# Performance work log

Hardware: AMD Instinct MI355X
Metric: run time of the kernel (lower is better)

## Reference

```python
import jax, jax.numpy as jnp
import numpy as np
import math

NUM_PARAM = 9
STRIDE = 1
BN_EPS = 1e-5


def _make_p_n(N):
    # matches LDConv._get_p_n: irregular kernel offset grid of N points
    base = round(math.sqrt(N))
    rows = N // base
    mod = N % base
    gx, gy = np.meshgrid(np.arange(rows), np.arange(base), indexing='ij')
    px, py = gx.ravel(), gy.ravel()
    if mod > 0:
        mx, my = np.meshgrid(np.arange(rows, rows + 1), np.arange(mod), indexing='ij')
        px = np.concatenate([px, mx.ravel()])
        py = np.concatenate([py, my.ravel()])
    return jnp.asarray(np.concatenate([px, py]), jnp.float32).reshape(1, 2 * N, 1, 1)


def _conv2d_same(x, w, stride, pad):
    return jax.lax.conv_general_dilated(
        x, w, (stride, stride), [(pad, pad), (pad, pad)],
        dimension_numbers=('NCHW', 'OIHW', 'NCHW'))


def _gather(xf, q, W, N):
    # xf: (b,c,H*W); q: (b,h,w,2N) int indices -> (b,c,h,w,N)
    idx = q[..., :N] * W + q[..., N:]
    return jax.vmap(lambda xb, ib: xb[:, ib])(xf, idx)


def setup_inputs() -> dict:
    key = jax.random.key(0)
    ks = jax.random.split(key, 3)
    B, C, H, W = 8, 128, 64, 64
    outc = 256
    x = jax.random.normal(ks[0], (B, C, H, W), jnp.float32)
    # p_conv init: uniform(-1e-4, 1e-4) weights, zero bias (per the torch module)
    p_conv_w = jax.random.uniform(ks[1], (2 * NUM_PARAM, C, 3, 3), jnp.float32, -1e-4, 1e-4)
    p_conv_b = jnp.zeros((2 * NUM_PARAM,), jnp.float32)
    conv_w = jax.random.normal(ks[2], (outc, C, NUM_PARAM, 1), jnp.float32) / math.sqrt(C * NUM_PARAM)
    bn_gamma = jnp.ones((outc,), jnp.float32)
    bn_beta = jnp.zeros((outc,), jnp.float32)
    bn_mean = jnp.zeros((outc,), jnp.float32)
    bn_var = jnp.ones((outc,), jnp.float32)
    return dict(x=x, p_conv_w=p_conv_w, p_conv_b=p_conv_b, conv_w=conv_w,
                bn_gamma=bn_gamma, bn_beta=bn_beta, bn_mean=bn_mean, bn_var=bn_var)


def reference(x, p_conv_w, p_conv_b, conv_w, bn_gamma, bn_beta, bn_mean, bn_var):
    N = NUM_PARAM
    B, C, H, W = x.shape
    offset = _conv2d_same(x, p_conv_w, STRIDE, 1) + p_conv_b[None, :, None, None]  # (b,2N,h,w)
    h, w = offset.shape[2], offset.shape[3]
    gx, gy = jnp.meshgrid(jnp.arange(0, h * STRIDE, STRIDE),
                          jnp.arange(0, w * STRIDE, STRIDE), indexing='ij')
    p_0 = jnp.concatenate([jnp.broadcast_to(gx, (1, N, h, w)),
                           jnp.broadcast_to(gy, (1, N, h, w))], axis=1).astype(x.dtype)
    p = (p_0 + _make_p_n(N) + offset).transpose(0, 2, 3, 1)  # (b,h,w,2N)

    q_lt = jnp.floor(jax.lax.stop_gradient(p))
    q_rb = q_lt + 1
    clampi = lambda q: jnp.concatenate([jnp.clip(q[..., :N], 0, H - 1),
                                        jnp.clip(q[..., N:], 0, W - 1)], -1).astype(jnp.int32)
    q_lt = clampi(q_lt)
    q_rb = clampi(q_rb)
    q_lb = jnp.concatenate([q_lt[..., :N], q_rb[..., N:]], -1)
    q_rt = jnp.concatenate([q_rb[..., :N], q_lt[..., N:]], -1)
    p = jnp.concatenate([jnp.clip(p[..., :N], 0, H - 1),
                         jnp.clip(p[..., N:], 0, W - 1)], -1)
    f = lambda q: q.astype(p.dtype)
    g_lt = (1 + (f(q_lt[..., :N]) - p[..., :N])) * (1 + (f(q_lt[..., N:]) - p[..., N:]))
    g_rb = (1 - (f(q_rb[..., :N]) - p[..., :N])) * (1 - (f(q_rb[..., N:]) - p[..., N:]))
    g_lb = (1 + (f(q_lb[..., :N]) - p[..., :N])) * (1 - (f(q_lb[..., N:]) - p[..., N:]))
    g_rt = (1 - (f(q_rt[..., :N]) - p[..., :N])) * (1 + (f(q_rt[..., N:]) - p[..., N:]))

    xf = x.reshape(B, C, H * W)
    x_off = (g_lt[:, None] * _gather(xf, q_lt, W, N)
             + g_rb[:, None] * _gather(xf, q_rb, W, N)
             + g_lb[:, None] * _gather(xf, q_lb, W, N)
             + g_rt[:, None] * _gather(xf, q_rt, W, N))  # (b,c,h,w,N)
    # rearrange 'b c h w n -> b c (h n) w'
    x_off = x_off.transpose(0, 1, 2, 4, 3).reshape(B, C, h * N, w)

    y = jax.lax.conv_general_dilated(x_off, conv_w, (N, 1), 'VALID',
                                     dimension_numbers=('NCHW', 'OIHW', 'NCHW'))
    scale = (bn_gamma / jnp.sqrt(bn_var + BN_EPS))[None, :, None, None]
    y = (y - bn_mean[None, :, None, None]) * scale + bn_beta[None, :, None, None]
    return y * jax.nn.sigmoid(y)  # SiLU
```

## Files before the change

kernel.cpp:

```cpp
#include <hip/hip_runtime.h>
#include <hip/hip_bf16.h>
#include <cstdint>

#define B_   8
#define C_   128
#define H_   64
#define W_   64
#define NPT  9
#define OC   256
#define K_   (C_*NPT)
#define HW   (H_*W_)
#define MTOT (B_*HW)

typedef __attribute__((ext_vector_type(8))) short short8;
typedef __attribute__((ext_vector_type(4))) float f32x4;
typedef __attribute__((ext_vector_type(4))) unsigned int u32x4;
typedef __attribute__((ext_vector_type(2))) unsigned int u32x2;

static __device__ __forceinline__ unsigned short f2bf(float f) {
    union { float f; unsigned u; } a; a.f = f;
    unsigned r = a.u + 0x7fffu + ((a.u >> 16) & 1u);
    return (unsigned short)(r >> 16);
}
static __device__ __forceinline__ float bf2f(unsigned short u) {
    union { unsigned u; float f; } a; a.u = ((unsigned)u) << 16;
    return a.f;
}

__global__ __launch_bounds__(512) void k_offset2(const float* __restrict__ x,
                                                 const float* __restrict__ pw,
                                                 const float* __restrict__ pb,
                                                 float* __restrict__ off) {
    __shared__ __align__(16) float wlds[128 * 180];
    __shared__ float red[8 * 64 * 19];
    int b = blockIdx.x >> 5;
    int i0 = (blockIdx.x & 31) * 2;
    int t = threadIdx.x;

    for (int idx = t; idx < 128 * 9 * 18; idx += 512) {
        int c = idx / 162;
        int r = idx - c * 162;
        int tap = r / 18;
        int o = r - tap * 18;
        wlds[c * 180 + tap * 20 + o] = pw[o * K_ + c * 9 + tap];
    }
    __syncthreads();

    int j = t & 63;
    int cg = t >> 6;
    const float* xb = x + (size_t)b * C_ * HW;
    float acc[2][18];
#pragma unroll
    for (int p = 0; p < 2; ++p)
#pragma unroll
        for (int o = 0; o < 18; ++o) acc[p][o] = 0.f;

    for (int cc = 0; cc < 16; ++cc) {
        int c = cg * 16 + cc;
        const float* xc = xb + (size_t)c * HW;
        float xv[4][3];
#pragma unroll
        for (int q = 0; q < 4; ++q) {
            int row = i0 - 1 + q;
            if (row >= 0 && row < H_) {
                const float* xr = xc + row * W_;
                xv[q][1] = xr[j];
                xv[q][0] = (j > 0)  ? xr[j - 1] : 0.f;
                xv[q][2] = (j < 63) ? xr[j + 1] : 0.f;
            } else {
                xv[q][0] = xv[q][1] = xv[q][2] = 0.f;
            }
        }
        const float* wc = wlds + c * 180;
#pragma unroll
        for (int tap = 0; tap < 9; ++tap) {
            const int kh = tap / 3, kw = tap % 3;
            float w18[20];
            *(f32x4*)(w18 + 0)  = *(const f32x4*)(wc + tap * 20 + 0);
            *(f32x4*)(w18 + 4)  = *(const f32x4*)(wc + tap * 20 + 4);
            *(f32x4*)(w18 + 8)  = *(const f32x4*)(wc + tap * 20 + 8);
            *(f32x4*)(w18 + 12) = *(const f32x4*)(wc + tap * 20 + 12);
            *(f32x4*)(w18 + 16) = *(const f32x4*)(wc + tap * 20 + 16);
#pragma unroll
            for (int p = 0; p < 2; ++p) {
                float xval = xv[p + kh][kw];
#pragma unroll
                for (int o = 0; o < 18; ++o) acc[p][o] += w18[o] * xval;
            }
        }
    }

#pragma unroll
    for (int p = 0; p < 2; ++p) {
        __syncthreads();
#pragma unroll
        for (int o = 0; o < 18; ++o) red[(cg * 64 + j) * 19 + o] = acc[p][o];
        __syncthreads();
        for (int e = t; e < 64 * 18; e += 512) {
            int jj = e / 18, o = e - jj * 18;
            float s = 0.f;
#pragma unroll
            for (int g = 0; g < 8; ++g) s += red[(g * 64 + jj) * 19 + o];
            off[(((size_t)b * 18 + o) * H_ + (i0 + p)) * W_ + jj] = s + pb[o];
        }
    }
}

__global__ __launch_bounds__(256) void k_prepw(const float* __restrict__ cw,
                                               const float* __restrict__ gam,
                                               const float* __restrict__ bet,
                                               const float* __restrict__ mu,
                                               const float* __restrict__ var,
                                               __hip_bfloat16* __restrict__ wbf,
                                               float* __restrict__ bias) {
    int idx = blockIdx.x * 256 + threadIdx.x;
    int oc = idx / K_;
    int r = idx - oc * K_;
    int n = r >> 7;
    int c = r & 127;
    float sc = gam[oc] * rsqrtf(var[oc] + 1e-5f);
    wbf[idx] = __float2bfloat16(cw[oc * K_ + c * NPT + n] * sc);
    if (blockIdx.x == 0 && threadIdx.x < OC) {
        int o = threadIdx.x;
        float s = gam[o] * rsqrtf(var[o] + 1e-5f);
        bias[o] = bet[o] - mu[o] * s;
    }
}

__global__ __launch_bounds__(256) void k_gather(const float* __restrict__ x,
                                                const float* __restrict__ off,
                                                __hip_bfloat16* __restrict__ xoff) {
    __shared__ __align__(16) char sx[98368 + 64];
    __shared__ __align__(16) f32x4 swt[1152];
    __shared__ uint32_t scrd[1152];
    int b = blockIdx.x >> 5;
    int i0 = (blockIdx.x & 31) * 2;
    int t = threadIdx.x;

    const float* xb = x + (size_t)b * C_ * HW;
#pragma unroll 4
    for (int it = 0; it < 48; ++it) {
        int q = it * 256 + t;
        int c = q / 96;
        int rem = q - c * 96;
        int s = rem >> 4;
        int c4 = rem & 15;
        int gr = min(63, max(0, i0 - 1 + s));
        f32x4 v = *(const f32x4*)(xb + (size_t)c * HW + gr * 64 + c4 * 4);
        u32x2 pk;
        pk.x = (uint32_t)f2bf(v.x) | ((uint32_t)f2bf(v.y) << 16);
        pk.y = (uint32_t)f2bf(v.z) | ((uint32_t)f2bf(v.w) << 16);
        *(u32x2*)(sx + c * 768 + ((c >> 6) << 6) + s * 128 + c4 * 8) = pk;
    }

    for (int task = t; task < 1152; task += 256) {
        int n = task >> 7;
        int pxl = task & 127;
        int i = i0 + (pxl >> 6);
        int j = pxl & 63;
        const float* ob = off + (((size_t)b * 18 + n) * H_ + i) * W_ + j;
        float ox = ob[0];
        float oy = ob[9 * HW];
        float pxf = (float)(i + n / 3) + ox;
        float pyf = (float)(j + n % 3) + oy;
        float fx = floorf(pxf), fy = floorf(pyf);
        int r0 = max(0, min(63, (int)fx));
        int r1 = max(0, min(63, (int)fx + 1));
        int c0 = max(0, min(63, (int)fy));
        int c1 = max(0, min(63, (int)fy + 1));
        float pxc = fminf(fmaxf(pxf, 0.f), 63.f);
        float pyc = fminf(fmaxf(pyf, 0.f), 63.f);
        float ax = 1.f + ((float)r0 - pxc);
        float bx = 1.f - ((float)r1 - pxc);
        float ay = 1.f + ((float)c0 - pyc);
        float by = 1.f - ((float)c1 - pyc);
        f32x4 w; w.x = ax * ay; w.y = bx * by; w.z = ax * by; w.w = bx * ay;
        swt[task] = w;
        int s0 = max(0, min(5, r0 - (i0 - 1)));
        int s1 = max(0, min(5, r1 - (i0 - 1)));
        scrd[task] = (uint32_t)(s0 | (s1 << 8) | (c0 << 16) | (c1 << 24));
    }
    __syncthreads();

    int wv = t >> 6;
    int h = (t >> 5) & 1;
    int pxl = wv * 32 + (t & 31);
    const char* sxh = sx + h * (64 * 768 + 64);
    char* ob = (char*)xoff + ((size_t)blockIdx.x * 128 + pxl) * (K_ * 2) + h * 128;
    for (int n = 0; n < 9; ++n) {
        f32x4 w = swt[n * 128 + pxl];
        uint32_t crd = scrd[n * 128 + pxl];
        int s0 = crd & 255, s1 = (crd >> 8) & 255, c0 = (crd >> 16) & 255, c1 = crd >> 24;
        int o00 = s0 * 128 + c0 * 2;
        int o11 = s1 * 128 + c1 * 2;
        int o01 = s0 * 128 + c1 * 2;
        int o10 = s1 * 128 + c0 * 2;
        for (int cg = 0; cg < 8; ++cg) {
            u32x4 pk;
#pragma unroll
            for (int u2 = 0; u2 < 4; ++u2) {
                unsigned short r[2];
#pragma unroll
                for (int e = 0; e < 2; ++e) {
                    int cl = cg * 8 + u2 * 2 + e;
                    const char* base = sxh + cl * 768;
                    float v = w.x * bf2f(*(const unsigned short*)(base + o00))
                            + w.y * bf2f(*(const unsigned short*)(base + o11))
                            + w.z * bf2f(*(const unsigned short*)(base + o01))
                            + w.w * bf2f(*(const unsigned short*)(base + o10));
                    r[e] = f2bf(v);
                }
                pk[u2] = (uint32_t)r[0] | ((uint32_t)r[1] << 16);
            }
            *(u32x4*)(ob + n * 256 + cg * 16) = pk;
        }
    }
}

#define BM 128
#define BN 128
#define BK 64
#define NTILES (K_ / BK)

__global__ __launch_bounds__(256) void k_gemm(const __hip_bfloat16* __restrict__ xoff,
                                              const __hip_bfloat16* __restrict__ wbf,
                                              const float* __restrict__ bias,
                                              float* __restrict__ out) {
    __shared__ __align__(16) char smem[2 * 2 * BM * BK * 2];
    int tid = threadIdx.x;
    int mt = blockIdx.x >> 1;
    int nt = blockIdx.x & 1;
    const char* Ab = (const char*)xoff + (size_t)mt * BM * (K_ * 2);
    const char* Bb = (const char*)wbf  + (size_t)nt * BN * (K_ * 2);

    auto stage = [&](int buf, int kt) {
        const int winByte = kt * (BK * 2);
#pragma unroll
        for (int q = 0; q < 4; ++q) {
            int ch = q * 256 + tid;
            int row = ch >> 3, slot = ch & 7;
            int srcoff = row * (K_ * 2) + winByte + ((slot * 16) ^ ((row & 7) << 4));
            __builtin_amdgcn_global_load_lds(
                (const __attribute__((address_space(1))) uint32_t*)(Ab + srcoff),
                (__attribute__((address_space(3))) uint32_t*)(smem + buf * 32768 + ch * 16),
                16, 0, 0);
        }
#pragma unroll
        for (int q = 0; q < 4; ++q) {
            int ch = q * 256 + tid;
            int row = ch >> 3, slot = ch & 7;
            int srcoff = row * (K_ * 2) + winByte + ((slot * 16) ^ ((row & 7) << 4));
            __builtin_amdgcn_global_load_lds(
                (const __attribute__((address_space(1))) uint32_t*)(Bb + srcoff),
                (__attribute__((address_space(3))) uint32_t*)(smem + buf * 32768 + 16384 + ch * 16),
                16, 0, 0);
        }
    };

    int wv = tid >> 6, lane = tid & 63;
    int wr = wv >> 1, wc = wv & 1;
    int lrow = lane & 15, lg = lane >> 4;

    f32x4 zero = {0.f, 0.f, 0.f, 0.f};
    f32x4 acc[4][4];
#pragma unroll
    for (int m = 0; m < 4; ++m)
#pragma unroll
        for (int n = 0; n < 4; ++n) acc[m][n] = zero;

    stage(0, 0);
    for (int kt = 0; kt < NTILES; ++kt) {
        if (kt + 1 < NTILES) stage((kt + 1) & 1, kt + 1);
        __syncthreads();
        const char* sa = smem + (kt & 1) * 32768;
        const char* sb = sa + 16384;
#pragma unroll
        for (int kk = 0; kk < 2; ++kk) {
            short8 afr[4], bfr[4];
#pragma unroll
            for (int m = 0; m < 4; ++m) {
                int row = wr * 64 + m * 16 + lrow;
                int byt = kk * 64 + lg * 16;
                afr[m] = *(const short8*)(sa + row * 128 + (byt ^ ((row & 7) << 4)));
            }
#pragma unroll
            for (int n = 0; n < 4; ++n) {
                int row = wc * 64 + n * 16 + lrow;
                int byt = kk * 64 + lg * 16;
                bfr[n] = *(const short8*)(sb + row * 128 + (byt ^ ((row & 7) << 4)));
            }
#pragma unroll
            for (int m = 0; m < 4; ++m)
#pragma unroll
                for (int n = 0; n < 4; ++n)
                    acc[m][n] = __builtin_amdgcn_mfma_f32_16x16x32_bf16(afr[m], bfr[n], acc[m][n], 0, 0, 0);
        }
        __syncthreads();
    }

#pragma unroll
    for (int n = 0; n < 4; ++n) {
        int oc = nt * BN + wc * 64 + n * 16 + lrow;
        float bs = bias[oc];
#pragma unroll
        for (int m = 0; m < 4; ++m) {
            int pxb = mt * BM + wr * 64 + m * 16 + lg * 4;
#pragma unroll
            for (int r = 0; r < 4; ++r) {
                int px = pxb + r;
                float v = acc[m][n][r] + bs;
                float sv = v / (1.f + __expf(-v));
                out[((size_t)(px >> 12) * OC + oc) * HW + (px & 4095)] = sv;
            }
        }
    }
}

extern "C" void kernel_launch(void* const* d_in, const int* in_sizes, int n_in,
                              void* d_out, int out_size, void* d_ws, size_t ws_size,
                              hipStream_t stream) {
    const float* x   = (const float*)d_in[0];
    const float* pw  = (const float*)d_in[1];
    const float* pb  = (const float*)d_in[2];
    const float* cw  = (const float*)d_in[3];
    const float* gam = (const float*)d_in[4];
    const float* bet = (const float*)d_in[5];
    const float* mu  = (const float*)d_in[6];
    const float* var = (const float*)d_in[7];
    float* out = (float*)d_out;

    char* ws = (char*)d_ws;
    float* off           = (float*)ws;
    __hip_bfloat16* wbf  = (__hip_bfloat16*)(ws + 2359296);
    float* bias          = (float*)(ws + 2949120);
    __hip_bfloat16* xoff = (__hip_bfloat16*)(ws + 2950144);

    hipLaunchKernelGGL(k_offset2, dim3(256),  dim3(512), 0, stream, x, pw, pb, off);
    hipLaunchKernelGGL(k_prepw,   dim3(1152), dim3(256), 0, stream, cw, gam, bet, mu, var, wbf, bias);
    hipLaunchKernelGGL(k_gather,  dim3(256),  dim3(256), 0, stream, x, off, xoff);
    hipLaunchKernelGGL(k_gemm,    dim3(512),  dim3(256), 0, stream, xoff, wbf, bias, out);
}
```

Measured before the change: 108.6 us.

## Restructure gather to channel-contiguous LDS layout and widen GEMM tile to full OC

The gather kernel now handles one output row per block and stores the 5-row input halo in LDS as pixel-major, channel-contiguous bf16 with an XOR swizzle. Each bilinear corner can then be read as 8-channel vector loads instead of scalar per-channel loads, and the per-pixel weights and coordinates stay in registers rather than going through LDS. The GEMM moves to 512-thread blocks covering all 256 output channels per 128-pixel tile, so each activation tile is loaded only once. The trade-off is fewer GEMM blocks (256), more LDS per block, and per-element scattered LDS stores when building the transposed halo.

```diff
diff --git a/kernel.cpp b/kernel.cpp
--- a/kernel.cpp
+++ b/kernel.cpp
@@ -130,39 +130,44 @@
 __global__ __launch_bounds__(256) void k_gather(const float* __restrict__ x,
                                                 const float* __restrict__ off,
                                                 __hip_bfloat16* __restrict__ xoff) {
-    __shared__ __align__(16) char sx[98368 + 64];
-    __shared__ __align__(16) f32x4 swt[1152];
-    __shared__ uint32_t scrd[1152];
-    int b = blockIdx.x >> 5;
-    int i0 = (blockIdx.x & 31) * 2;
+    __shared__ __align__(16) char sx[5 * 64 * 256];
+    int b = blockIdx.x >> 6;
+    int i = blockIdx.x & 63;
     int t = threadIdx.x;
 
     const float* xb = x + (size_t)b * C_ * HW;
 #pragma unroll 4
-    for (int it = 0; it < 48; ++it) {
-        int q = it * 256 + t;
-        int c = q / 96;
-        int rem = q - c * 96;
-        int s = rem >> 4;
-        int c4 = rem & 15;
-        int gr = min(63, max(0, i0 - 1 + s));
+    for (int it = 0; it < 40; ++it) {
+        int ch = it * 256 + t;
+        int c4 = ch & 15;
+        int c  = (ch >> 4) & 127;
+        int s  = ch >> 11;
+        int gr = min(63, max(0, i - 1 + s));
         f32x4 v = *(const f32x4*)(xb + (size_t)c * HW + gr * 64 + c4 * 4);
-        u32x2 pk;
-        pk.x = (uint32_t)f2bf(v.x) | ((uint32_t)f2bf(v.y) << 16);
-        pk.y = (uint32_t)f2bf(v.z) | ((uint32_t)f2bf(v.w) << 16);
-        *(u32x2*)(sx + c * 768 + ((c >> 6) << 6) + s * 128 + c4 * 8) = pk;
-    }
-
-    for (int task = t; task < 1152; task += 256) {
-        int n = task >> 7;
-        int pxl = task & 127;
-        int i = i0 + (pxl >> 6);
-        int j = pxl & 63;
-        const float* ob = off + (((size_t)b * 18 + n) * H_ + i) * W_ + j;
-        float ox = ob[0];
-        float oy = ob[9 * HW];
-        float pxf = (float)(i + n / 3) + ox;
-        float pyf = (float)(j + n % 3) + oy;
+        int g = c >> 3;
+        int sub = (c & 7) * 2;
+#pragma unroll
+        for (int k2 = 0; k2 < 4; ++k2) {
+            int col = c4 * 4 + k2;
+            *(unsigned short*)(sx + (s * 64 + col) * 256 + (((g ^ (col & 15)) << 4) + sub)) = f2bf(v[k2]);
+        }
+    }
+
+    int j = t & 63;
+    int cg = t >> 6;
+    float oxv[9], oyv[9];
+    const float* ob = off + (((size_t)b * 18) * H_ + i) * W_ + j;
+#pragma unroll
+    for (int n = 0; n < 9; ++n) {
+        oxv[n] = ob[(size_t)n * HW];
+        oyv[n] = ob[(size_t)(n + 9) * HW];
+    }
+    __syncthreads();
+
+    char* outp = (char*)xoff + ((size_t)blockIdx.x * 64 + j) * (K_ * 2) + cg * 64;
+    for (int n = 0; n < 9; ++n) {
+        float pxf = (float)(i + n / 3) + oxv[n];
+        float pyf = (float)(j + n % 3) + oyv[n];
         float fx = floorf(pxf), fy = floorf(pyf);
         int r0 = max(0, min(63, (int)fx));
         int r1 = max(0, min(63, (int)fx + 1));
@@ -174,91 +179,81 @@
         float bx = 1.f - ((float)r1 - pxc);
         float ay = 1.f + ((float)c0 - pyc);
         float by = 1.f - ((float)c1 - pyc);
-        f32x4 w; w.x = ax * ay; w.y = bx * by; w.z = ax * by; w.w = bx * ay;
-        swt[task] = w;
-        int s0 = max(0, min(5, r0 - (i0 - 1)));
-        int s1 = max(0, min(5, r1 - (i0 - 1)));
-        scrd[task] = (uint32_t)(s0 | (s1 << 8) | (c0 << 16) | (c1 << 24));
-    }
-    __syncthreads();
-
-    int wv = t >> 6;
-    int h = (t >> 5) & 1;
-    int pxl = wv * 32 + (t & 31);
-    const char* sxh = sx + h * (64 * 768 + 64);
-    char* ob = (char*)xoff + ((size_t)blockIdx.x * 128 + pxl) * (K_ * 2) + h * 128;
-    for (int n = 0; n < 9; ++n) {
-        f32x4 w = swt[n * 128 + pxl];
-        uint32_t crd = scrd[n * 128 + pxl];
-        int s0 = crd & 255, s1 = (crd >> 8) & 255, c0 = (crd >> 16) & 255, c1 = crd >> 24;
-        int o00 = s0 * 128 + c0 * 2;
-        int o11 = s1 * 128 + c1 * 2;
-        int o01 = s0 * 128 + c1 * 2;
-        int o10 = s1 * 128 + c0 * 2;
-        for (int cg = 0; cg < 8; ++cg) {
+        float w00 = ax * ay, w11 = bx * by, w01 = ax * by, w10 = bx * ay;
+        int s0 = max(0, min(4, r0 - (i - 1)));
+        int s1 = max(0, min(4, r1 - (i - 1)));
+        const char* b00 = sx + (s0 * 64 + c0) * 256;
+        const char* b11 = sx + (s1 * 64 + c1) * 256;
+        const char* b01 = sx + (s0 * 64 + c1) * 256;
+        const char* b10 = sx + (s1 * 64 + c0) * 256;
+        int x0m = (c0 & 15) << 4, x1m = (c1 & 15) << 4;
+#pragma unroll
+        for (int u = 0; u < 4; ++u) {
+            int gb = (cg * 4 + u) << 4;
+            short8 t00 = *(const short8*)(b00 + (gb ^ x0m));
+            short8 t11 = *(const short8*)(b11 + (gb ^ x1m));
+            short8 t01 = *(const short8*)(b01 + (gb ^ x1m));
+            short8 t10 = *(const short8*)(b10 + (gb ^ x0m));
             u32x4 pk;
 #pragma unroll
-            for (int u2 = 0; u2 < 4; ++u2) {
-                unsigned short r[2];
+            for (int p2 = 0; p2 < 4; ++p2) {
+                unsigned short rr[2];
 #pragma unroll
                 for (int e = 0; e < 2; ++e) {
-                    int cl = cg * 8 + u2 * 2 + e;
-                    const char* base = sxh + cl * 768;
-                    float v = w.x * bf2f(*(const unsigned short*)(base + o00))
-                            + w.y * bf2f(*(const unsigned short*)(base + o11))
-                            + w.z * bf2f(*(const unsigned short*)(base + o01))
-                            + w.w * bf2f(*(const unsigned short*)(base + o10));
-                    r[e] = f2bf(v);
+                    int ei = p2 * 2 + e;
+                    float v = w00 * bf2f((unsigned short)t00[ei])
+                            + w11 * bf2f((unsigned short)t11[ei])
+                            + w01 * bf2f((unsigned short)t01[ei])
+                            + w10 * bf2f((unsigned short)t10[ei]);
+                    rr[e] = f2bf(v);
                 }
-                pk[u2] = (uint32_t)r[0] | ((uint32_t)r[1] << 16);
-            }
-            *(u32x4*)(ob + n * 256 + cg * 16) = pk;
-        }
-    }
-}
-
-#define BM 128
-#define BN 128
-#define BK 64
-#define NTILES (K_ / BK)
-
-__global__ __launch_bounds__(256) void k_gemm(const __hip_bfloat16* __restrict__ xoff,
+                pk[p2] = (uint32_t)rr[0] | ((uint32_t)rr[1] << 16);
+            }
+            *(u32x4*)(outp + n * 256 + u * 16) = pk;
+        }
+    }
+}
+
+#define GBM 128
+#define GBN 256
+#define GBK 64
+#define NT_G (K_ / GBK)
+
+__global__ __launch_bounds__(512) void k_gemm(const __hip_bfloat16* __restrict__ xoff,
                                               const __hip_bfloat16* __restrict__ wbf,
                                               const float* __restrict__ bias,
                                               float* __restrict__ out) {
-    __shared__ __align__(16) char smem[2 * 2 * BM * BK * 2];
+    __shared__ __align__(16) char smem[2 * (16384 + 32768)];
     int tid = threadIdx.x;
-    int mt = blockIdx.x >> 1;
-    int nt = blockIdx.x & 1;
-    const char* Ab = (const char*)xoff + (size_t)mt * BM * (K_ * 2);
-    const char* Bb = (const char*)wbf  + (size_t)nt * BN * (K_ * 2);
+    int mt = blockIdx.x;
+    const char* Ab = (const char*)xoff + (size_t)mt * GBM * (K_ * 2);
+    const char* Bb = (const char*)wbf;
 
     auto stage = [&](int buf, int kt) {
-        const int winByte = kt * (BK * 2);
-#pragma unroll
-        for (int q = 0; q < 4; ++q) {
-            int ch = q * 256 + tid;
+        const int winByte = kt * (GBK * 2);
+        char* base = smem + buf * 49152;
+#pragma unroll
+        for (int q = 0; q < 2; ++q) {
+            int ch = q * 512 + tid;
             int row = ch >> 3, slot = ch & 7;
             int srcoff = row * (K_ * 2) + winByte + ((slot * 16) ^ ((row & 7) << 4));
             __builtin_amdgcn_global_load_lds(
                 (const __attribute__((address_space(1))) uint32_t*)(Ab + srcoff),
-                (__attribute__((address_space(3))) uint32_t*)(smem + buf * 32768 + ch * 16),
-                16, 0, 0);
+                (__attribute__((address_space(3))) uint32_t*)(base + ch * 16), 16, 0, 0);
         }
 #pragma unroll
         for (int q = 0; q < 4; ++q) {
-            int ch = q * 256 + tid;
+            int ch = q * 512 + tid;
             int row = ch >> 3, slot = ch & 7;
             int srcoff = row * (K_ * 2) + winByte + ((slot * 16) ^ ((row & 7) << 4));
             __builtin_amdgcn_global_load_lds(
                 (const __attribute__((address_space(1))) uint32_t*)(Bb + srcoff),
-                (__attribute__((address_space(3))) uint32_t*)(smem + buf * 32768 + 16384 + ch * 16),
-                16, 0, 0);
+                (__attribute__((address_space(3))) uint32_t*)(base + 16384 + ch * 16), 16, 0, 0);
         }
     };
 
     int wv = tid >> 6, lane = tid & 63;
-    int wr = wv >> 1, wc = wv & 1;
+    int wr = wv >> 2, wc = wv & 3;
     int lrow = lane & 15, lg = lane >> 4;
 
     f32x4 zero = {0.f, 0.f, 0.f, 0.f};
@@ -269,10 +264,10 @@
         for (int n = 0; n < 4; ++n) acc[m][n] = zero;
 
     stage(0, 0);
-    for (int kt = 0; kt < NTILES; ++kt) {
-        if (kt + 1 < NTILES) stage((kt + 1) & 1, kt + 1);
+    for (int kt = 0; kt < NT_G; ++kt) {
+        if (kt + 1 < NT_G) stage((kt + 1) & 1, kt + 1);
         __syncthreads();
-        const char* sa = smem + (kt & 1) * 32768;
+        const char* sa = smem + (kt & 1) * 49152;
         const char* sb = sa + 16384;
 #pragma unroll
         for (int kk = 0; kk < 2; ++kk) {
@@ -300,11 +295,11 @@
 
 #pragma unroll
     for (int n = 0; n < 4; ++n) {
-        int oc = nt * BN + wc * 64 + n * 16 + lrow;
+        int oc = wc * 64 + n * 16 + lrow;
         float bs = bias[oc];
 #pragma unroll
         for (int m = 0; m < 4; ++m) {
-            int pxb = mt * BM + wr * 64 + m * 16 + lg * 4;
+            int pxb = mt * GBM + wr * 64 + m * 16 + lg * 4;
 #pragma unroll
             for (int r = 0; r < 4; ++r) {
                 int px = pxb + r;
@@ -337,6 +332,6 @@
 
     hipLaunchKernelGGL(k_offset2, dim3(256),  dim3(512), 0, stream, x, pw, pb, off);
     hipLaunchKernelGGL(k_prepw,   dim3(1152), dim3(256), 0, stream, cw, gam, bet, mu, var, wbf, bias);
-    hipLaunchKernelGGL(k_gather,  dim3(256),  dim3(256), 0, stream, x, off, xoff);
-    hipLaunchKernelGGL(k_gemm,    dim3(512),  dim3(256), 0, stream, xoff, wbf, bias, out);
-}
+    hipLaunchKernelGGL(k_gather,  dim3(512),  dim3(256), 0, stream, x, off, xoff);
+    hipLaunchKernelGGL(k_gemm,    dim3(256),  dim3(512), 0, stream, xoff, wbf, bias, out);
+}
```

Result: no change. 108.6 us (+0.0%).
